# Optimization experiments

Measured on AMD Instinct MI355X. Metric: run time of the kernel, lower is better.

Reference implementation:

```python
import jax, jax.numpy as jnp
import numpy as np

DIM = 1024


def setup_inputs() -> dict:
    key = jax.random.key(0)
    kx, kw = jax.random.split(key)
    x = jax.random.normal(kx, (4, 2048, DIM), dtype=jnp.float32)
    # fused qkv projection weight, torch Linear convention: [out_features, in_features]
    W_qkv = jax.random.normal(kw, (3 * DIM, DIM), dtype=jnp.float32) * (DIM ** -0.5)
    return {"x": x, "W_qkv": W_qkv}


def reference(x, W_qkv):
    # fused QKV projection: y = x @ W^T -> [B, N, 3*DIM]
    qkv = jnp.einsum('bnd,ed->bne', x, W_qkv)
    B, N, _ = qkv.shape
    # rearrange 'b n (e d) -> e b n d' with e=3
    qkv = qkv.reshape(B, N, 3, DIM).transpose(2, 0, 1, 3)
    q, k, v = qkv[0], qkv[1], qkv[2]
    scale = DIM ** (-0.5)  # note: scale uses full dim, module never splits heads
    attn = jnp.einsum('bnd,bmd->bnm', q * scale, k)  # [B, N, N]
    attn = jax.nn.softmax(attn, axis=-1)
    out = jnp.einsum('bnm,bmd->bnd', attn, v)
    return out
```

## Files before the change

kernel.cpp:

```cpp
#include <hip/hip_runtime.h>

using half8   = __attribute__((ext_vector_type(8))) _Float16;
using f32x4   = __attribute__((ext_vector_type(4))) float;
using ushort8 = __attribute__((ext_vector_type(8))) unsigned short;

__device__ __forceinline__ void gload16(const void* g, void* l) {
  __builtin_amdgcn_global_load_lds(
      (const __attribute__((address_space(1))) void*)g,
      (__attribute__((address_space(3))) void*)l, 16, 0, 0);
}

__device__ __forceinline__ void xcd_swizzle(int& x, int& y, int& z) {
  const int gx = gridDim.x, gy = gridDim.y;
  const int nwg = gx * gy * gridDim.z;
  const int f = blockIdx.x + gx * (blockIdx.y + gy * blockIdx.z);
  const int w = (f & 7) * (nwg >> 3) + (f >> 3);
  const int r = w >> 5, u = w & 31;
  const int nrx = gx >> 3, nry = gy >> 2;
  const int pz  = nrx * nry;
  const int rz  = r / pz, rr = r % pz;
  x = (rr % nrx) * 8 + (u & 7);
  y = (rr / nrx) * 4 + (u >> 3);
  z = rz;
}

__global__ __launch_bounds__(256) void cast_f32_f16(
    const float* __restrict__ in, unsigned short* __restrict__ out, long n) {
  long i = ((long)blockIdx.x * 256 + threadIdx.x) * 8;
  if (i >= n) return;
  float4 a = *(const float4*)(in + i);
  float4 b = *(const float4*)(in + i + 4);
  union { _Float16 h[8]; ushort8 u; } r;
  r.h[0] = (_Float16)a.x; r.h[1] = (_Float16)a.y;
  r.h[2] = (_Float16)a.z; r.h[3] = (_Float16)a.w;
  r.h[4] = (_Float16)b.x; r.h[5] = (_Float16)b.y;
  r.h[6] = (_Float16)b.z; r.h[7] = (_Float16)b.w;
  *(ushort8*)(out + i) = r.u;
}

template <int MODE>
__global__ __launch_bounds__(256, 2) void gemm4w(
    const unsigned short* __restrict__ Ab, const unsigned short* __restrict__ Bb,
    int K, int lda, int ldb, long sA, long sB,
    void* __restrict__ o0, void* __restrict__ o1, void* __restrict__ o2) {
  constexpr int ASZ = 128 * 64;
  constexpr int BSZ = 128 * 64;
  __shared__ unsigned short lds[2 * ASZ + 2 * BSZ];

  const int tid  = threadIdx.x;
  const int lane = tid & 63;
  const int wv   = tid >> 6;
  const int wr   = wv >> 1, wc = wv & 1;
  const int fr   = lane & 15, fq = lane >> 4;
  int bxi, byi, bzi;
  xcd_swizzle(bxi, byi, bzi);
  const int bm = byi * 128;
  const int bn = bxi * 128;
  const int bz = bzi;

  const unsigned short* A = Ab + (long)bz * sA;
  const unsigned short* B = Bb + (long)bz * sB;

  const int row_s = tid >> 3;
  const int col_s = ((tid & 7) ^ (row_s & 7)) * 8;
  const unsigned short* aS = A + (long)(bm + row_s) * lda + col_s;
  const unsigned short* bS = B + (long)(bn + row_s) * ldb + col_s;
  unsigned short* ldsA = lds;
  unsigned short* ldsB = lds + 2 * ASZ;

  const int kg0 = ((0 * 4 + fq) ^ (fr & 7)) * 16;
  const int kg1 = ((1 * 4 + fq) ^ (fr & 7)) * 16;
  const int aRd = (wr * 64 + fr) * 128;
  const int bRd = (wc * 64 + fr) * 128;

  f32x4 acc[4][4] = {};
  half8 bf[4][2];
  half8 a0[2], a1[2], a2[2], a3[2];

  const int nt = K / 64;

#define STAGE_T(SL, T)                                                             \
  {                                                                                \
    const long kt = (long)(T) * 64;                                                \
    unsigned short* dA = ldsA + (SL) * ASZ + wv * 512;                             \
    unsigned short* dB = ldsB + (SL) * BSZ + wv * 512;                             \
    _Pragma("unroll") for (int i = 0; i < 4; ++i)                                  \
      gload16(aS + (long)(i * 32) * lda + kt, dA + i * 2048);                      \
    _Pragma("unroll") for (int i = 0; i < 4; ++i)                                  \
      gload16(bS + (long)(i * 32) * ldb + kt, dB + i * 2048);                      \
  }
#define RDA(DST, MI)                                                               \
  DST[0] = *(const half8*)(lA + aRd + (MI) * 2048 + kg0);                          \
  DST[1] = *(const half8*)(lA + aRd + (MI) * 2048 + kg1);
#define MFMAQ(MI, AA)                                                              \
  __builtin_amdgcn_s_setprio(1);                                                   \
  _Pragma("unroll") for (int ks = 0; ks < 2; ++ks)                                 \
  _Pragma("unroll") for (int ni = 0; ni < 4; ++ni)                                 \
    acc[MI][ni] = __builtin_amdgcn_mfma_f32_16x16x32_f16(                          \
        AA[ks], bf[ni][ks], acc[MI][ni], 0, 0, 0);                                 \
  __builtin_amdgcn_s_setprio(0);

  STAGE_T(0, 0)
  asm volatile("s_waitcnt vmcnt(0)" ::: "memory");
  __builtin_amdgcn_s_barrier();
  __builtin_amdgcn_sched_barrier(0);

  for (int tt = 0; tt < nt; ++tt) {
    const int sl = tt & 1;
    const char* lA = (const char*)(ldsA + sl * ASZ);
    const char* lB = (const char*)(ldsB + sl * BSZ);
#pragma unroll
    for (int ni = 0; ni < 4; ++ni) {
      bf[ni][0] = *(const half8*)(lB + bRd + ni * 2048 + kg0);
      bf[ni][1] = *(const half8*)(lB + bRd + ni * 2048 + kg1);
    }
    RDA(a0, 0)
    RDA(a1, 1)
    if (tt + 1 < nt) STAGE_T(sl ^ 1, tt + 1)
    MFMAQ(0, a0)
    RDA(a2, 2)
    MFMAQ(1, a1)
    RDA(a3, 3)
    MFMAQ(2, a2)
    MFMAQ(3, a3)
    asm volatile("s_waitcnt vmcnt(0)" ::: "memory");
    __builtin_amdgcn_s_barrier();
    __builtin_amdgcn_sched_barrier(0);
  }
#undef STAGE_T
#undef RDA
#undef MFMAQ

  const int row0 = bm + wr * 64 + fq * 4;
  const int col0 = bn + wc * 64 + fr;
#pragma unroll
  for (int mi = 0; mi < 4; ++mi) {
#pragma unroll
    for (int ni = 0; ni < 4; ++ni) {
      f32x4 c = acc[mi][ni];
      const long r0 = row0 + mi * 16;
      const long e  = col0 + ni * 16;
      if constexpr (MODE == 0) {
        _Float16* q  = (_Float16*)o0;
        _Float16* kk = (_Float16*)o1;
        _Float16* vv = (_Float16*)o2;
#pragma unroll
        for (int j = 0; j < 4; ++j) {
          const long i = r0 + j;
          const float val = c[j];
          if (e < 1024)      q [i * 1024 + e]          = (_Float16)(val * 0.03125f);
          else if (e < 2048) kk[i * 1024 + (e - 1024)] = (_Float16)val;
          else               vv[i * 1024 + (e - 2048)] = (_Float16)val;
        }
      } else if constexpr (MODE == 1) {
        _Float16* C = (_Float16*)o0 + (long)bz * 2048 * 2048;
#pragma unroll
        for (int j = 0; j < 4; ++j) C[(r0 + j) * 2048 + e] = (_Float16)c[j];
      } else {
        float* C = (float*)o0 + (long)bz * 2048 * 1024;
#pragma unroll
        for (int j = 0; j < 4; ++j) C[(r0 + j) * 1024 + e] = c[j];
      }
    }
  }
}

__global__ __launch_bounds__(256) void transpose_v(
    const unsigned short* __restrict__ v, unsigned short* __restrict__ vT) {
  __shared__ unsigned short t[64][72];
  const long b = blockIdx.z;
  const unsigned short* vb = v + b * (2048L * 1024);
  unsigned short* ob = vT + b * (1024L * 2048);
  const int n0 = blockIdx.y * 64;
  const int d0 = blockIdx.x * 64;
  const int tid = threadIdx.x;
  const int r  = tid >> 2;
  const int c0 = (tid & 3) * 16;
  const unsigned short* src = vb + (long)(n0 + r) * 1024 + d0 + c0;
  *(ushort4*)&t[r][c0]      = *(const ushort4*)(src);
  *(ushort4*)&t[r][c0 + 4]  = *(const ushort4*)(src + 4);
  *(ushort4*)&t[r][c0 + 8]  = *(const ushort4*)(src + 8);
  *(ushort4*)&t[r][c0 + 12] = *(const ushort4*)(src + 12);
  __syncthreads();
  union { unsigned short h[8]; ushort8 u; } w0, w1;
#pragma unroll
  for (int j = 0; j < 8; ++j) w0.h[j] = t[c0 + j][r];
#pragma unroll
  for (int j = 0; j < 8; ++j) w1.h[j] = t[c0 + 8 + j][r];
  unsigned short* dst = ob + (long)(d0 + r) * 2048 + n0 + c0;
  *(ushort8*)dst       = w0.u;
  *(ushort8*)(dst + 8) = w1.u;
}

__global__ __launch_bounds__(256) void softmax_rows_f16(unsigned short* __restrict__ S) {
  const long row = blockIdx.x;
  unsigned short* p = S + row * 2048;
  const int t = threadIdx.x;
  union { ushort8 u; _Float16 h[8]; } in;
  in.u = *(const ushort8*)(p + t * 8);
  float f[8];
#pragma unroll
  for (int j = 0; j < 8; ++j) f[j] = (float)in.h[j];
  float m = f[0];
#pragma unroll
  for (int j = 1; j < 8; ++j) m = fmaxf(m, f[j]);
  for (int o = 32; o; o >>= 1) m = fmaxf(m, __shfl_xor(m, o));
  __shared__ float redm[4];
  if (!(t & 63)) redm[t >> 6] = m;
  __syncthreads();
  m = fmaxf(fmaxf(redm[0], redm[1]), fmaxf(redm[2], redm[3]));
  float e[8], s = 0.f;
#pragma unroll
  for (int j = 0; j < 8; ++j) { e[j] = __expf(f[j] - m); s += e[j]; }
  for (int o = 32; o; o >>= 1) s += __shfl_xor(s, o);
  __shared__ float reds[4];
  if (!(t & 63)) reds[t >> 6] = s;
  __syncthreads();
  s = reds[0] + reds[1] + reds[2] + reds[3];
  const float inv = 1.0f / s;
  union { _Float16 h[8]; ushort8 u; } r;
#pragma unroll
  for (int j = 0; j < 8; ++j) r.h[j] = (_Float16)(e[j] * inv);
  *(ushort8*)(p + t * 8) = r.u;
}

extern "C" void kernel_launch(void* const* d_in, const int* in_sizes, int n_in,
                              void* d_out, int out_size, void* d_ws, size_t ws_size,
                              hipStream_t stream) {
  const float* x = (const float*)d_in[0];
  const float* W = (const float*)d_in[1];
  float* out = (float*)d_out;
  char* ws = (char*)d_ws;

  const long MB = 1048576;
  unsigned short* q   = (unsigned short*)(ws);
  unsigned short* k   = (unsigned short*)(ws + 16 * MB);
  unsigned short* vT  = (unsigned short*)(ws + 32 * MB);
  unsigned short* S16 = (unsigned short*)(ws + 48 * MB);
  unsigned short* xb = (unsigned short*)(ws + 48 * MB);
  unsigned short* wb = (unsigned short*)(ws + 64 * MB);
  unsigned short* v  = (unsigned short*)(ws + 70 * MB);

  cast_f32_f16<<<4096, 256, 0, stream>>>(x, xb, 8388608L);
  cast_f32_f16<<<1536, 256, 0, stream>>>(W, wb, 3145728L);
  gemm4w<0><<<dim3(24, 64, 1), 256, 0, stream>>>(
      xb, wb, 1024, 1024, 1024, 0L, 0L, q, k, v);
  transpose_v<<<dim3(16, 32, 4), 256, 0, stream>>>(v, vT);
  gemm4w<1><<<dim3(16, 16, 4), 256, 0, stream>>>(
      q, k, 1024, 1024, 1024, 2048L * 1024, 2048L * 1024, S16, nullptr, nullptr);
  softmax_rows_f16<<<8192, 256, 0, stream>>>(S16);
  gemm4w<2><<<dim3(8, 16, 4), 256, 0, stream>>>(
      S16, vT, 2048, 2048, 2048, 2048L * 2048, 1024L * 2048,
      out, nullptr, nullptr);
}
```

Measured before the change: 166.8 us.

## Fuse x cast into QKV GEMM and write V transposed from epilogue

Adds a dedicated QKV projection kernel that loads x in fp32 straight from global memory, converts it to fp16 in registers and writes it into LDS. This removes the separate x cast kernel and its fp16 intermediate. The epilogue writes V directly in transposed layout, which removes the transpose kernel and one extra pass over V. In exchange, the A operand now goes through registers instead of async global-to-LDS loads, which adds register pressure and latency, and the transposed V stores are strided 8-byte writes.

```diff
diff --git a/kernel.cpp b/kernel.cpp
--- a/kernel.cpp
+++ b/kernel.cpp
@@ -38,11 +38,160 @@
   *(ushort8*)(out + i) = r.u;
 }
 
+__global__ __launch_bounds__(256, 2) void gemm_qkv(
+    const float* __restrict__ X, const unsigned short* __restrict__ Wb,
+    unsigned short* __restrict__ q, unsigned short* __restrict__ kk,
+    unsigned short* __restrict__ vT) {
+  constexpr int ASZ = 128 * 64;
+  constexpr int BSZ = 128 * 64;
+  __shared__ unsigned short lds[2 * ASZ + 2 * BSZ];
+
+  const int tid  = threadIdx.x;
+  const int lane = tid & 63;
+  const int wv   = tid >> 6;
+  const int wr   = wv >> 1, wc = wv & 1;
+  const int fr   = lane & 15, fq = lane >> 4;
+  int bxi, byi, bzi;
+  xcd_swizzle(bxi, byi, bzi);
+  const int bm = byi * 128;
+  const int bn = bxi * 128;
+
+  const int row_s = tid >> 3;
+  const int col_s = ((tid & 7) ^ (row_s & 7)) * 8;
+  const unsigned short* bS = Wb + (long)(bn + row_s) * 1024 + col_s;
+  unsigned short* ldsA = lds;
+  unsigned short* ldsB = lds + 2 * ASZ;
+
+  const int arow = tid >> 3;
+  const int ag   = tid & 7;
+  const float* aS = X + (long)(bm + arow) * 1024 + ag * 8;
+  const int awr = arow * 64 + ((ag ^ (arow & 7)) * 8);
+
+  const int kg0 = ((0 * 4 + fq) ^ (fr & 7)) * 16;
+  const int kg1 = ((1 * 4 + fq) ^ (fr & 7)) * 16;
+  const int aRd = (wr * 64 + fr) * 128;
+  const int bRd = (wc * 64 + fr) * 128;
+
+  f32x4 acc[4][4] = {};
+  half8 bf[4][2];
+  half8 a0[2], a1[2], a2[2], a3[2];
+  float4 fA[4][2];
+
+  const int nt = 1024 / 64;
+
+#define LOAD_A(T)                                                                  \
+  {                                                                                \
+    const long kt = (long)(T) * 64;                                                \
+    _Pragma("unroll") for (int p = 0; p < 4; ++p) {                                \
+      fA[p][0] = *(const float4*)(aS + (long)p * 32 * 1024 + kt);                  \
+      fA[p][1] = *(const float4*)(aS + (long)p * 32 * 1024 + kt + 4);              \
+    }                                                                              \
+  }
+#define WRITE_A(SL)                                                                \
+  {                                                                                \
+    unsigned short* d = ldsA + (SL) * ASZ + awr;                                   \
+    _Pragma("unroll") for (int p = 0; p < 4; ++p) {                                \
+      union { _Float16 h[8]; ushort8 u; } w;                                       \
+      w.h[0] = (_Float16)fA[p][0].x; w.h[1] = (_Float16)fA[p][0].y;                \
+      w.h[2] = (_Float16)fA[p][0].z; w.h[3] = (_Float16)fA[p][0].w;                \
+      w.h[4] = (_Float16)fA[p][1].x; w.h[5] = (_Float16)fA[p][1].y;                \
+      w.h[6] = (_Float16)fA[p][1].z; w.h[7] = (_Float16)fA[p][1].w;                \
+      *(ushort8*)(d + p * 2048) = w.u;                                             \
+    }                                                                              \
+  }
+#define STAGE_B(SL, T)                                                             \
+  {                                                                                \
+    const long kt = (long)(T) * 64;                                                \
+    unsigned short* d = ldsB + (SL) * BSZ + wv * 512;                              \
+    _Pragma("unroll") for (int i = 0; i < 4; ++i)                                  \
+      gload16(bS + (long)(i * 32) * 1024 + kt, d + i * 2048);                      \
+  }
+#define RDA(DST, MI)                                                               \
+  DST[0] = *(const half8*)(lA + aRd + (MI) * 2048 + kg0);                          \
+  DST[1] = *(const half8*)(lA + aRd + (MI) * 2048 + kg1);
+#define MFMAQ(MI, AA)                                                              \
+  __builtin_amdgcn_s_setprio(1);                                                   \
+  _Pragma("unroll") for (int ks = 0; ks < 2; ++ks)                                 \
+  _Pragma("unroll") for (int ni = 0; ni < 4; ++ni)                                 \
+    acc[MI][ni] = __builtin_amdgcn_mfma_f32_16x16x32_f16(                          \
+        AA[ks], bf[ni][ks], acc[MI][ni], 0, 0, 0);                                 \
+  __builtin_amdgcn_s_setprio(0);
+
+  LOAD_A(0)
+  STAGE_B(0, 0)
+  WRITE_A(0)
+  asm volatile("s_waitcnt vmcnt(0) lgkmcnt(0)" ::: "memory");
+  __builtin_amdgcn_s_barrier();
+  __builtin_amdgcn_sched_barrier(0);
+
+  for (int tt = 0; tt < nt; ++tt) {
+    const int sl = tt & 1;
+    const char* lA = (const char*)(ldsA + sl * ASZ);
+    const char* lB = (const char*)(ldsB + sl * BSZ);
+#pragma unroll
+    for (int ni = 0; ni < 4; ++ni) {
+      bf[ni][0] = *(const half8*)(lB + bRd + ni * 2048 + kg0);
+      bf[ni][1] = *(const half8*)(lB + bRd + ni * 2048 + kg1);
+    }
+    RDA(a0, 0)
+    RDA(a1, 1)
+    if (tt + 1 < nt) {
+      LOAD_A(tt + 1)
+      STAGE_B(sl ^ 1, tt + 1)
+    }
+    MFMAQ(0, a0)
+    RDA(a2, 2)
+    MFMAQ(1, a1)
+    RDA(a3, 3)
+    MFMAQ(2, a2)
+    MFMAQ(3, a3)
+    if (tt + 1 < nt) WRITE_A(sl ^ 1)
+    asm volatile("s_waitcnt vmcnt(0) lgkmcnt(0)" ::: "memory");
+    __builtin_amdgcn_s_barrier();
+    __builtin_amdgcn_sched_barrier(0);
+  }
+#undef LOAD_A
+#undef WRITE_A
+#undef STAGE_B
+#undef RDA
+#undef MFMAQ
+
+  const int row0 = bm + wr * 64 + fq * 4;
+  const int col0 = bn + wc * 64 + fr;
+#pragma unroll
+  for (int mi = 0; mi < 4; ++mi) {
+#pragma unroll
+    for (int ni = 0; ni < 4; ++ni) {
+      f32x4 c = acc[mi][ni];
+      const long r0 = row0 + mi * 16;
+      const long e  = col0 + ni * 16;
+      if (e < 1024) {
+        _Float16* qq = (_Float16*)q;
+#pragma unroll
+        for (int j = 0; j < 4; ++j)
+          qq[(r0 + j) * 1024 + e] = (_Float16)(c[j] * 0.03125f);
+      } else if (e < 2048) {
+        _Float16* kp = (_Float16*)kk;
+#pragma unroll
+        for (int j = 0; j < 4; ++j)
+          kp[(r0 + j) * 1024 + (e - 1024)] = (_Float16)c[j];
+      } else {
+        const long d = e - 2048;
+        const long b = r0 >> 11;
+        const long n = r0 & 2047;
+        union { _Float16 h[4]; ushort4 u; } w4;
+#pragma unroll
+        for (int j = 0; j < 4; ++j) w4.h[j] = (_Float16)c[j];
+        *(ushort4*)(vT + b * (1024L * 2048) + d * 2048 + n) = w4.u;
+      }
+    }
+  }
+}
+
 template <int MODE>
 __global__ __launch_bounds__(256, 2) void gemm4w(
     const unsigned short* __restrict__ Ab, const unsigned short* __restrict__ Bb,
-    int K, int lda, int ldb, long sA, long sB,
-    void* __restrict__ o0, void* __restrict__ o1, void* __restrict__ o2) {
+    int K, int lda, int ldb, long sA, long sB, void* __restrict__ o0) {
   constexpr int ASZ = 128 * 64;
   constexpr int BSZ = 128 * 64;
   __shared__ unsigned short lds[2 * ASZ + 2 * BSZ];
@@ -140,19 +289,7 @@
       f32x4 c = acc[mi][ni];
       const long r0 = row0 + mi * 16;
       const long e  = col0 + ni * 16;
-      if constexpr (MODE == 0) {
-        _Float16* q  = (_Float16*)o0;
-        _Float16* kk = (_Float16*)o1;
-        _Float16* vv = (_Float16*)o2;
-#pragma unroll
-        for (int j = 0; j < 4; ++j) {
-          const long i = r0 + j;
-          const float val = c[j];
-          if (e < 1024)      q [i * 1024 + e]          = (_Float16)(val * 0.03125f);
-          else if (e < 2048) kk[i * 1024 + (e - 1024)] = (_Float16)val;
-          else               vv[i * 1024 + (e - 2048)] = (_Float16)val;
-        }
-      } else if constexpr (MODE == 1) {
+      if constexpr (MODE == 1) {
         _Float16* C = (_Float16*)o0 + (long)bz * 2048 * 2048;
 #pragma unroll
         for (int j = 0; j < 4; ++j) C[(r0 + j) * 2048 + e] = (_Float16)c[j];
@@ -163,33 +300,6 @@
       }
     }
   }
-}
-
-__global__ __launch_bounds__(256) void transpose_v(
-    const unsigned short* __restrict__ v, unsigned short* __restrict__ vT) {
-  __shared__ unsigned short t[64][72];
-  const long b = blockIdx.z;
-  const unsigned short* vb = v + b * (2048L * 1024);
-  unsigned short* ob = vT + b * (1024L * 2048);
-  const int n0 = blockIdx.y * 64;
-  const int d0 = blockIdx.x * 64;
-  const int tid = threadIdx.x;
-  const int r  = tid >> 2;
-  const int c0 = (tid & 3) * 16;
-  const unsigned short* src = vb + (long)(n0 + r) * 1024 + d0 + c0;
-  *(ushort4*)&t[r][c0]      = *(const ushort4*)(src);
-  *(ushort4*)&t[r][c0 + 4]  = *(const ushort4*)(src + 4);
-  *(ushort4*)&t[r][c0 + 8]  = *(const ushort4*)(src + 8);
-  *(ushort4*)&t[r][c0 + 12] = *(const ushort4*)(src + 12);
-  __syncthreads();
-  union { unsigned short h[8]; ushort8 u; } w0, w1;
-#pragma unroll
-  for (int j = 0; j < 8; ++j) w0.h[j] = t[c0 + j][r];
-#pragma unroll
-  for (int j = 0; j < 8; ++j) w1.h[j] = t[c0 + 8 + j][r];
-  unsigned short* dst = ob + (long)(d0 + r) * 2048 + n0 + c0;
-  *(ushort8*)dst       = w0.u;
-  *(ushort8*)(dst + 8) = w1.u;
 }
 
 __global__ __launch_bounds__(256) void softmax_rows_f16(unsigned short* __restrict__ S) {
@@ -237,19 +347,13 @@
   unsigned short* k   = (unsigned short*)(ws + 16 * MB);
   unsigned short* vT  = (unsigned short*)(ws + 32 * MB);
   unsigned short* S16 = (unsigned short*)(ws + 48 * MB);
-  unsigned short* xb = (unsigned short*)(ws + 48 * MB);
-  unsigned short* wb = (unsigned short*)(ws + 64 * MB);
-  unsigned short* v  = (unsigned short*)(ws + 70 * MB);
-
-  cast_f32_f16<<<4096, 256, 0, stream>>>(x, xb, 8388608L);
+  unsigned short* wb  = (unsigned short*)(ws + 80 * MB);
+
   cast_f32_f16<<<1536, 256, 0, stream>>>(W, wb, 3145728L);
-  gemm4w<0><<<dim3(24, 64, 1), 256, 0, stream>>>(
-      xb, wb, 1024, 1024, 1024, 0L, 0L, q, k, v);
-  transpose_v<<<dim3(16, 32, 4), 256, 0, stream>>>(v, vT);
+  gemm_qkv<<<dim3(24, 64, 1), 256, 0, stream>>>(x, wb, q, k, vT);
   gemm4w<1><<<dim3(16, 16, 4), 256, 0, stream>>>(
-      q, k, 1024, 1024, 1024, 2048L * 1024, 2048L * 1024, S16, nullptr, nullptr);
+      q, k, 1024, 1024, 1024, 2048L * 1024, 2048L * 1024, S16);
   softmax_rows_f16<<<8192, 256, 0, stream>>>(S16);
   gemm4w<2><<<dim3(8, 16, 4), 256, 0, stream>>>(
-      S16, vT, 2048, 2048, 2048, 2048L * 2048, 1024L * 2048,
-      out, nullptr, nullptr);
-}
+      S16, vT, 2048, 2048, 2048, 2048L * 2048, 1024L * 2048, out);
+}
```

Result: slower. 178.2 us (+6.8%).
